# Kernel tuning notes

Measured on AMD Instinct MI355X. Metric: run time of the kernel, lower is better.

Reference implementation:

```python
import jax, jax.numpy as jnp
import numpy as np

EPS = 1e-8

def _rasterize_mesh(face_verts, H, W):
    # face_verts: [F,3,3] = (ndc_x, ndc_y, view_z) per triangle vertex
    x0, y0, z0 = face_verts[:, 0, 0], face_verts[:, 0, 1], face_verts[:, 0, 2]
    x1, y1, z1 = face_verts[:, 1, 0], face_verts[:, 1, 1], face_verts[:, 1, 2]
    x2, y2, z2 = face_verts[:, 2, 0], face_verts[:, 2, 1], face_verts[:, 2, 2]
    area = (x1 - x0) * (y2 - y0) - (y1 - y0) * (x2 - x0)
    # cull_backfaces=True (area<=0) + degenerate + behind-camera cull
    face_ok = (area > EPS) & (z0 > 0) & (z1 > 0) & (z2 > 0)
    inv_area = jnp.where(face_ok, 1.0 / jnp.where(face_ok, area, 1.0), 0.0)
    zs = jnp.stack([z0, z1, z2], -1)  # [F,3]
    # pytorch3d NDC: +x left, +y up, pixel centers
    xs = 1.0 - (2.0 * jnp.arange(W, dtype=jnp.float32) + 1.0) / W
    ys = 1.0 - (2.0 * jnp.arange(H, dtype=jnp.float32) + 1.0) / H

    def row_fn(py):
        px = xs[:, None]  # [W,1] broadcast vs faces [F]
        w0 = ((x1 - px) * (y2 - py) - (y1 - py) * (x2 - px)) * inv_area
        w1 = ((x2 - px) * (y0 - py) - (y2 - py) * (x0 - px)) * inv_area
        w2 = ((x0 - px) * (y1 - py) - (y0 - py) * (x1 - px)) * inv_area
        inside = (w0 >= 0) & (w1 >= 0) & (w2 >= 0) & face_ok
        # perspective_correct=True: l_i = w_i * prod(other z), renormalize
        l = jnp.stack([w0 * z1 * z2, z0 * w1 * z2, z0 * z1 * w2], -1)  # [W,F,3]
        s = l.sum(-1, keepdims=True)
        b = l / jnp.where(s == 0, 1.0, s)
        # clip_barycentric_coords=True
        b = jnp.clip(b, 0.0, None)
        b = b / jnp.clip(b.sum(-1, keepdims=True), EPS, None)
        zpix = (b * zs[None]).sum(-1)  # [W,F] interpolated view-space depth
        zm = jnp.where(inside, zpix, jnp.inf)
        fidx = jnp.argmin(zm, axis=1)  # z-buffer winner per pixel
        zmin = jnp.take_along_axis(zm, fidx[:, None], 1)[:, 0]
        hit = jnp.isfinite(zmin)
        bary = jnp.take_along_axis(b, fidx[:, None, None], 1)[:, 0]  # [W,3]
        return (jnp.where(hit, fidx, -1),
                jnp.where(hit, zmin, -1.0),
                jnp.where(hit[:, None], bary, -1.0))

    return jax.lax.map(row_fn, ys)  # ([H,W],[H,W],[H,W,3])


def _forward(positions, features, faces, K, RT, H, W):
    B, V, _ = positions.shape
    Fn = faces.shape[1]
    # --- create_camera_objects: open3d/opencv KRT -> pytorch3d camera ---
    R = RT[:, :, :3]
    t = RT[:, :, 3]
    scale = min(H, W) / 2.0
    focal = jnp.stack([K[:, 0, 0], K[:, 1, 1]], -1) / scale  # [B,2] NDC focal
    p0 = -(jnp.stack([K[:, 0, 2], K[:, 1, 2]], -1)
           - jnp.array([W / 2.0, H / 2.0], jnp.float32)) / scale  # [B,2]
    sign = jnp.array([-1.0, -1.0, 1.0], jnp.float32)
    R_p = jnp.swapaxes(R, 1, 2) * sign[None, None, :]  # R^T with cols 0,1 negated
    T_p = t * sign[None, :]
    # --- _get_mesh_ndc: world -> view -> NDC (pytorch3d row-vector convention) ---
    v_view = jnp.einsum('bvi,bij->bvj', positions, R_p) + T_p[:, None, :]
    z = v_view[..., 2:3]
    xy_ndc = focal[:, None, :] * v_view[..., :2] / z + p0[:, None, :]
    verts_ndc = jnp.concatenate([xy_ndc, z], -1)  # z overwritten with view-space depth
    face_verts = jax.vmap(lambda v, f: v[f])(verts_ndc, faces)  # [B,F,3,3]
    # --- rasterize (blur_sigma=0 -> faces_per_pixel=1) ---
    p2f, zbuf, bary = jax.vmap(lambda fv: _rasterize_mesh(fv, H, W))(face_verts)
    hit = p2f >= 0
    pix_to_face = jnp.where(hit, p2f + (jnp.arange(B) * Fn)[:, None, None], -1)
    # --- interpolate_face_attributes on packed faces/verts ---
    faces_packed = (faces + (jnp.arange(B) * V)[:, None, None]).reshape(B * Fn, 3)
    feats_packed = features.reshape(B * V, -1)
    fv_idx = faces_packed[jnp.clip(pix_to_face, 0)]  # [B,H,W,3]
    attrs = feats_packed[fv_idx]                      # [B,H,W,3,C]
    pix_feats = (bary[..., None] * attrs).sum(-2)
    pix_feats = jnp.where(hit[..., None], pix_feats, 0.0)
    dists = jnp.where(hit, 0.0, -1.0)
    # add faces_per_pixel (K=1) axis, matching pytorch3d Fragments layout
    return (pix_feats[:, :, :, None, :], pix_to_face[:, :, :, None],
            zbuf[:, :, :, None], bary[:, :, :, None, :], dists[:, :, :, None])


def setup_inputs() -> dict:
    key = jax.random.key(0)
    k1, k2, k3 = jax.random.split(key, 3)
    B, V, Fn, C, H, W = 1, 8192, 16384, 64, 192, 192
    positions = jax.random.uniform(k1, (B, V, 3), jnp.float32) * 2.0 - 1.0
    features = jax.random.normal(k2, (B, V, C), jnp.float32)
    faces = jax.random.randint(k3, (B, Fn, 3), 0, V)
    K = jnp.broadcast_to(jnp.array([[180.0, 0.0, 96.0], [0.0, 180.0, 96.0],
                                    [0.0, 0.0, 1.0]], jnp.float32), (B, 3, 3))
    RT = jnp.broadcast_to(jnp.concatenate(
        [jnp.eye(3, dtype=jnp.float32),
         jnp.array([[0.0], [0.0], [3.5]], jnp.float32)], axis=1), (B, 3, 4))
    return {"positions": positions, "features": features, "faces": faces,
            "K": K, "RT": RT, "H": H, "W": W, "blur_sigma": 0}


def reference(positions, features, faces, K, RT, H, W, blur_sigma):
    # blur_sigma == 0 path of VertexShader.forward (faces_per_pixel=1)
    return _forward(positions, features, faces, K, RT, H, W)
```

## Files before the change

kernel.cpp:

```cpp
#include <hip/hip_runtime.h>
#include <stdint.h>

#define H_ 192
#define W_ 192
#define C_ 64
#define EPS_F 1e-8f
#define TILE 16
#define NTX (W_/TILE)
#define NTY (H_/TILE)
#define CHUNK 256
#define NSLICE 8
#define NBUCKET 256
#define MAXCHUNK 64

typedef unsigned long long ull;

#define OFF_FEATS 0
#define OFF_P2F   (H_*W_*C_)
#define OFF_ZBUF  (OFF_P2F + H_*W_)
#define OFF_BARY  (OFF_ZBUF + H_*W_)
#define OFF_DIST  (OFF_BARY + H_*W_*3)

__device__ __forceinline__ float xm(float a, float b){ return __fmul_rn(a,b); }
__device__ __forceinline__ float xa(float a, float b){ return __fadd_rn(a,b); }
__device__ __forceinline__ float xsb(float a, float b){ return __fsub_rn(a,b); }
__device__ __forceinline__ float xd(float a, float b){ return __fdiv_rn(a,b); }

__device__ __forceinline__ float pixcoord(int i, float dim){
    float t = xa(xm(2.0f, (float)i), 1.0f);
    return xsb(1.0f, xd(t, dim));
}

__device__ __forceinline__ unsigned fenc(float f){
    unsigned b = __float_as_uint(f);
    return (b & 0x80000000u) ? ~b : (b | 0x80000000u);
}
__device__ __forceinline__ float fdec(unsigned e){
    unsigned b = (e & 0x80000000u) ? (e & 0x7FFFFFFFu) : ~e;
    return __uint_as_float(b);
}

__device__ __forceinline__ int zbucket(float zmn){
    int b = (int)((zmn - 2.0f) * 64.0f);
    return b < 0 ? 0 : (b > 254 ? 254 : b);
}
__device__ __forceinline__ float zlo_bucket(int b){
    if (b >= 255) return INFINITY;
    if (b == 0)   return 0.0f;
    return 2.0f + (float)b * 0.015625f;
}

__device__ __forceinline__ float3 tv(const float* __restrict__ pos,
        const float* __restrict__ K, const float* __restrict__ RT, int i){
    float p0 = pos[3*i+0], p1 = pos[3*i+1], p2 = pos[3*i+2];
    const float sgn[3] = {-1.f, -1.f, 1.f};
    float vv[3];
    #pragma unroll
    for (int j=0;j<3;j++){
        float rp0 = xm(RT[j*4+0], sgn[j]);
        float rp1 = xm(RT[j*4+1], sgn[j]);
        float rp2 = xm(RT[j*4+2], sgn[j]);
        float s = xa(xa(xm(p0,rp0), xm(p1,rp1)), xm(p2,rp2));
        vv[j] = xa(s, xm(RT[j*4+3], sgn[j]));
    }
    float z = vv[2];
    float fx = xd(K[0], 96.0f);
    float fy = xd(K[4], 96.0f);
    float p0x = -xd(xsb(K[2], 96.0f), 96.0f);
    float p0y = -xd(xsb(K[5], 96.0f), 96.0f);
    float xn = xa(xd(xm(fx, vv[0]), z), p0x);
    float yn = xa(xd(xm(fy, vv[1]), z), p0y);
    return make_float3(xn, yn, z);
}

__global__ __launch_bounds__(64) void k_pre(const float* __restrict__ pos,
        const float* __restrict__ K, const float* __restrict__ RT,
        const int* __restrict__ faces, float* __restrict__ rec0,
        unsigned* __restrict__ hist, unsigned* __restrict__ gbb,
        ull* __restrict__ keys, int Fn){
    __shared__ unsigned lh[NBUCKET];
    int t = threadIdx.x, B = blockIdx.x;
    int gthreads = gridDim.x*64;
    for (int i = B*64 + t; i < H_*W_; i += gthreads) keys[i] = 0xFFFFFFFFFFFFFFFFULL;
    #pragma unroll
    for (int i=t; i<NBUCKET; i+=64) lh[i] = 0u;
    __syncthreads();
    int f = B*64 + t;
    float bxmn=INFINITY, bxmx=-INFINITY, bymn=INFINITY, bymx=-INFINITY;
    if (f < Fn){
        int i0 = faces[3*f+0], i1 = faces[3*f+1], i2 = faces[3*f+2];
        float3 v0 = tv(pos,K,RT,i0), v1 = tv(pos,K,RT,i1), v2 = tv(pos,K,RT,i2);
        float area = xsb(xm(xsb(v1.x,v0.x), xsb(v2.y,v0.y)), xm(xsb(v1.y,v0.y), xsb(v2.x,v0.x)));
        bool ok = (area > EPS_F) && (v0.z > 0.f) && (v1.z > 0.f) && (v2.z > 0.f);
        float ia = ok ? xd(1.0f, area) : 0.0f;
        float zmn = INFINITY;
        int b = 255;
        if (ok){
            zmn = fminf(v0.z, fminf(v1.z, v2.z));
            b = zbucket(zmn);
            bxmn = fminf(v0.x, fminf(v1.x, v2.x)) - 1e-4f;
            bxmx = fmaxf(v0.x, fmaxf(v1.x, v2.x)) + 1e-4f;
            bymn = fminf(v0.y, fminf(v1.y, v2.y)) - 1e-4f;
            bymx = fmaxf(v0.y, fmaxf(v1.y, v2.y)) + 1e-4f;
        }
        atomicAdd(&lh[b], 1u);
        float4* q = (float4*)(rec0 + (size_t)f*12);
        q[0] = make_float4(v0.x, v0.y, v1.x, v1.y);
        q[1] = make_float4(v2.x, v2.y, v0.z, v1.z);
        q[2] = make_float4(v2.z, ia, __int_as_float(f), zmn);
    }
    #pragma unroll
    for (int s2=1; s2<64; s2<<=1){
        bxmn = fminf(bxmn, __shfl_xor(bxmn, s2, 64));
        bxmx = fmaxf(bxmx, __shfl_xor(bxmx, s2, 64));
        bymn = fminf(bymn, __shfl_xor(bymn, s2, 64));
        bymx = fmaxf(bymx, __shfl_xor(bymx, s2, 64));
    }
    if (t == 0 && bxmx > -INFINITY){
        atomicMax(&gbb[0], fenc(-bxmn));
        atomicMax(&gbb[1], fenc( bxmx));
        atomicMax(&gbb[2], fenc(-bymn));
        atomicMax(&gbb[3], fenc( bymx));
    }
    __syncthreads();
    #pragma unroll
    for (int i=t; i<NBUCKET; i+=64){
        unsigned cc = lh[i];
        if (cc) atomicAdd(&hist[i], cc);
    }
}

__global__ __launch_bounds__(256) void k_scatter(const float* __restrict__ rec0,
        const unsigned* __restrict__ hist, unsigned* __restrict__ histcur,
        float* __restrict__ rec, float* __restrict__ suffz, int Fn){
    __shared__ unsigned gst[NBUCKET], ssc[NBUCKET], lcnt[NBUCKET], lbase[NBUCKET];
    int t = threadIdx.x, B = blockIdx.x;
    unsigned hv = hist[t];
    ssc[t] = hv;
    lcnt[t] = 0u;
    __syncthreads();
    for (int d=1; d<NBUCKET; d<<=1){
        unsigned u = (t >= d) ? ssc[t-d] : 0u;
        __syncthreads();
        ssc[t] += u;
        __syncthreads();
    }
    gst[t] = ssc[t] - hv;
    __syncthreads();
    if (B == 0 && t < MAXCHUNK){
        unsigned pos = (unsigned)t * CHUNK;
        int bb = 0;
        #pragma unroll
        for (int s = 128; s > 0; s >>= 1){
            int nb = bb + s;
            if (nb <= NBUCKET && ssc[nb-1] <= pos) bb = nb;
        }
        suffz[t] = zlo_bucket(bb);
    }
    int f = B*256 + t;
    bool valid = (f < Fn);
    float4 q0, q1, q2;
    int b = 255; unsigned rank = 0; bool ok = false; float zmn = INFINITY;
    if (valid){
        const float4* q = (const float4*)(rec0 + (size_t)f*12);
        q0 = q[0]; q1 = q[1]; q2 = q[2];
        ok = (q2.y > 0.f);
        zmn = q2.w;
        b = ok ? zbucket(zmn) : 255;
        rank = atomicAdd(&lcnt[b], 1u);
    }
    __syncthreads();
    unsigned add = lcnt[t];
    if (add) lbase[t] = atomicAdd(&histcur[t], add);
    __syncthreads();
    if (valid){
        float x0=q0.x, y0=q0.y, x1=q0.z, y1=q0.w;
        float x2=q1.x, y2=q1.y, z0=q1.z, z1=q1.w;
        float z2=q2.x, ia=q2.y;
        float xmn, xmx, ymn, ymx, Ap=0.f, Bp=0.f, Cp=0.f;
        if (ok){
            xmn = fminf(x0, fminf(x1, x2)) - 1e-4f;
            xmx = fmaxf(x0, fmaxf(x1, x2)) + 1e-4f;
            ymn = fminf(y0, fminf(y1, y2)) - 1e-4f;
            ymx = fmaxf(y0, fmaxf(y1, y2)) + 1e-4f;
            float iz0 = 1.f/z0, iz1 = 1.f/z1, iz2 = 1.f/z2;
            Ap = ia * ((y1-y2)*iz0 + (y2-y0)*iz1 + (y0-y1)*iz2);
            Bp = ia * ((x2-x1)*iz0 + (x0-x2)*iz1 + (x1-x0)*iz2);
            Cp = ia * ((x1*y2-x2*y1)*iz0 + (x2*y0-x0*y2)*iz1 + (x0*y1-x1*y0)*iz2);
        } else {
            xmn = INFINITY; xmx = -INFINITY; ymn = INFINITY; ymx = -INFINITY;
        }
        unsigned p = gst[b] + lbase[b] + rank;
        float4* qo = (float4*)(rec + (size_t)p*20);
        qo[0] = q0; qo[1] = q1; qo[2] = q2;
        qo[3] = make_float4(Ap, Bp, Cp, 0.f);
        qo[4] = make_float4(xmn, xmx, ymn, ymx);
    }
}

__global__ __launch_bounds__(256) void k_raster(const float* __restrict__ rec,
        const float* __restrict__ suffz, const unsigned* __restrict__ gbb,
        ull* __restrict__ keys, int Fn){
    __shared__ float lds[CHUNK*12];
    __shared__ float zl[CHUNK];
    __shared__ int   slist[CHUNK];
    __shared__ int   wcnt[4];
    __shared__ float suff[MAXCHUNK];
    int tid = threadIdx.x;
    int nchunk = (Fn + CHUNK - 1) / CHUNK;
    if (tid < MAXCHUNK) suff[tid] = suffz[tid];
    int ix = blockIdx.x*TILE + (tid & 15);
    int iy = blockIdx.y*TILE + (tid >> 4);
    int pix = iy*W_ + ix;
    float px = pixcoord(ix, (float)W_);
    float py = pixcoord(iy, (float)H_);
    float tx_hi = pixcoord(blockIdx.x*TILE,          (float)W_);
    float tx_lo = pixcoord(blockIdx.x*TILE + TILE-1, (float)W_);
    float ty_hi = pixcoord(blockIdx.y*TILE,          (float)H_);
    float ty_lo = pixcoord(blockIdx.y*TILE + TILE-1, (float)H_);
    float gx0 = -fdec(gbb[0]), gx1 = fdec(gbb[1]);
    float gy0 = -fdec(gbb[2]), gy1 = fdec(gbb[3]);
    bool alive = (px >= gx0) && (px <= gx1) && (py >= gy0) && (py <= gy1);
    int lane = tid & 63, wv = tid >> 6;

    float zcut = alive ? INFINITY : -INFINITY;
    ull localkey = 0xFFFFFFFFFFFFFFFFULL;
    ull published = 0xFFFFFFFFFFFFFFFFULL;
    __syncthreads();

    for (int c = (int)blockIdx.z; c < nchunk; c += NSLICE){
        ull g = __hip_atomic_load(&keys[pix], __ATOMIC_RELAXED, __HIP_MEMORY_SCOPE_AGENT);
        float zg = __uint_as_float((unsigned)(g >> 32));
        zcut = fminf(zcut, zg);
        float sc = (c < MAXCHUNK) ? suff[c] : 0.0f;
        int done = (!alive || !(xm(sc, 0.999f) < zcut)) ? 1 : 0;
        if (__syncthreads_and(done)) break;

        int fi = c*CHUNK + tid;
        float4 q0 = make_float4(0,0,0,0), q1 = q0, q2 = q0;
        bool keep = false;
        float zb = 0.f;
        if (fi < Fn){
            const float4* gq = (const float4*)(rec + (size_t)fi*20);
            q0 = gq[0]; q1 = gq[1]; q2 = gq[2];
            float4 q3 = gq[3], q4 = gq[4];
            keep = (q4.x <= tx_hi) && (q4.y >= tx_lo) && (q4.z <= ty_hi) && (q4.w >= ty_lo);
            if (keep){
                float ax = (q3.x > 0.f) ? tx_hi : tx_lo;
                float by = (q3.y > 0.f) ? ty_hi : ty_lo;
                float Nmax = q3.z + q3.x*ax + q3.y*by;
                float M = fabsf(q3.x*ax) + fabsf(q3.y*by) + fabsf(q3.z);
                float Nub = Nmax + 1e-5f*M + 1e-30f;
                if (Nub <= 0.f) keep = false;
                else zb = fmaxf(1.f/Nub, q2.w);
            }
        }
        float4* l = (float4*)(lds + tid*12);
        l[0] = q0; l[1] = q1; l[2] = q2;
        ull m = __ballot(keep);
        if (lane == 0) wcnt[wv] = __popcll(m);
        __syncthreads();
        int basecnt = 0;
        #pragma unroll
        for (int w2 = 0; w2 < 4; ++w2) if (w2 < wv) basecnt += wcnt[w2];
        if (keep){
            int p = basecnt + __popcll(m & ((1ULL << lane) - 1ULL));
            slist[p] = tid;
            zl[p] = zb;
        }
        int nsurv = wcnt[0] + wcnt[1] + wcnt[2] + wcnt[3];
        __syncthreads();

        float zcmax = zcut;
        #pragma unroll
        for (int s2=1; s2<64; s2<<=1) zcmax = fmaxf(zcmax, __shfl_xor(zcmax, s2, 64));

        for (int k0 = 0; k0 < nsurv; k0 += 64){
            int kk = k0 + lane;
            float zlk = (kk < nsurv) ? zl[kk] : INFINITY;
            ull wm = __ballot(xm(zlk, 0.999f) < zcmax);
            while (wm){
                int k = (int)__ffsll(wm) - 1;
                wm &= wm - 1;
                k += k0;
                float zbl = zl[k];
                if (xm(zbl, 0.999f) < zcut){
                    int j = slist[k];
                    const float* r = lds + j*12;
                    float x0=r[0], y0=r[1], x1=r[2], y1=r[3], x2=r[4], y2=r[5];
                    float dx0=xsb(x0,px), dx1=xsb(x1,px), dx2=xsb(x2,px);
                    float dy0=xsb(y0,py), dy1=xsb(y1,py), dy2=xsb(y2,py);
                    float e0 = xsb(xm(dx1,dy2), xm(dy1,dx2));
                    float e1 = xsb(xm(dx2,dy0), xm(dy2,dx0));
                    float e2 = xsb(xm(dx0,dy1), xm(dy0,dx1));
                    if (e0 >= 0.f && e1 >= 0.f && e2 >= 0.f){
                        float z0=r[6], z1=r[7], z2=r[8], ia=r[9];
                        float w0 = xm(e0, ia), w1 = xm(e1, ia), w2 = xm(e2, ia);
                        float l0 = xm(xm(w0,z1),z2);
                        float l1 = xm(xm(z0,w1),z2);
                        float l2 = xm(xm(z0,z1),w2);
                        float s  = xa(xa(l0,l1),l2);
                        float za = (l0*z0 + l1*z1 + l2*z2) / s;
                        if (za*0.99999f < zcut){
                            float dn = (s == 0.f) ? 1.0f : s;
                            float b0 = fmaxf(xd(l0,dn), 0.f);
                            float b1 = fmaxf(xd(l1,dn), 0.f);
                            float b2 = fmaxf(xd(l2,dn), 0.f);
                            float bs = fmaxf(xa(xa(b0,b1),b2), EPS_F);
                            b0 = xd(b0,bs); b1 = xd(b1,bs); b2 = xd(b2,bs);
                            float zp = xa(xa(xm(b0,z0),xm(b1,z1)),xm(b2,z2));
                            ull ck = (((ull)__float_as_uint(zp)) << 32) | (unsigned)__float_as_int(r[10]);
                            if (ck < localkey) localkey = ck;
                            zcut = fminf(zcut, zp);
                        }
                    }
                }
            }
        }
        if (localkey < published){
            atomicMin(&keys[pix], localkey);
            published = localkey;
        }
    }
    if (localkey < published) atomicMin(&keys[pix], localkey);
}

__global__ __launch_bounds__(256) void k_post(const ull* __restrict__ keys,
        const float* __restrict__ rec0, const float* __restrict__ feats,
        const int* __restrict__ faces, float* __restrict__ out){
    int grp = threadIdx.x >> 6;
    int c = threadIdx.x & 63;
    int pix = blockIdx.x*4 + grp;
    float* p2f  = out + OFF_P2F;
    float* zbuf = out + OFF_ZBUF;
    float* bary = out + OFF_BARY;
    float* dist = out + OFF_DIST;
    ull key = keys[pix];
    if (key == 0xFFFFFFFFFFFFFFFFULL){
        out[OFF_FEATS + pix*C_ + c] = 0.0f;
        if (c == 0){
            p2f[pix] = -1.0f; zbuf[pix] = -1.0f; dist[pix] = -1.0f;
        }
        if (c < 3) bary[3*pix+c] = -1.0f;
        return;
    }
    int f = (int)(key & 0xFFFFFFFFu);
    float z = __uint_as_float((unsigned)(key >> 32));
    int ix = pix % W_, iy = pix / W_;
    float px = pixcoord(ix, (float)W_);
    float py = pixcoord(iy, (float)H_);
    const float4* q = (const float4*)(rec0 + (size_t)f*12);
    float4 q0 = q[0], q1 = q[1], q2 = q[2];
    float x0=q0.x, y0=q0.y, x1=q0.z, y1=q0.w;
    float x2=q1.x, y2=q1.y, z0=q1.z, z1=q1.w;
    float z2=q2.x, ia=q2.y;
    float w0 = xm(xsb(xm(xsb(x1,px),xsb(y2,py)), xm(xsb(y1,py),xsb(x2,px))), ia);
    float w1 = xm(xsb(xm(xsb(x2,px),xsb(y0,py)), xm(xsb(y2,py),xsb(x0,px))), ia);
    float w2 = xm(xsb(xm(xsb(x0,px),xsb(y1,py)), xm(xsb(y0,py),xsb(x1,px))), ia);
    float l0 = xm(xm(w0,z1),z2);
    float l1 = xm(xm(z0,w1),z2);
    float l2 = xm(xm(z0,z1),w2);
    float s  = xa(xa(l0,l1),l2);
    float dn = (s == 0.f) ? 1.0f : s;
    float b0 = fmaxf(xd(l0,dn), 0.f);
    float b1 = fmaxf(xd(l1,dn), 0.f);
    float b2 = fmaxf(xd(l2,dn), 0.f);
    float bs = fmaxf(xa(xa(b0,b1),b2), EPS_F);
    b0 = xd(b0,bs); b1 = xd(b1,bs); b2 = xd(b2,bs);
    int i0 = faces[3*f+0], i1 = faces[3*f+1], i2 = faces[3*f+2];
    float res = xa(xa(xm(b0, feats[i0*C_ + c]), xm(b1, feats[i1*C_ + c])),
                   xm(b2, feats[i2*C_ + c]));
    out[OFF_FEATS + pix*C_ + c] = res;
    if (c == 0){
        p2f[pix] = (float)f; zbuf[pix] = z; dist[pix] = 0.0f;
    }
    if (c < 3){
        float bb = (c == 0) ? b0 : ((c == 1) ? b1 : b2);
        bary[3*pix+c] = bb;
    }
}

extern "C" void kernel_launch(void* const* d_in, const int* in_sizes, int n_in,
                              void* d_out, int out_size, void* d_ws, size_t ws_size,
                              hipStream_t stream) {
    const float* positions = (const float*)d_in[0];
    const float* features  = (const float*)d_in[1];
    const int*   faces     = (const int*)  d_in[2];
    const float* K         = (const float*)d_in[3];
    const float* RT        = (const float*)d_in[4];
    int Fn = in_sizes[2] / 3;

    ull*      keys     = (ull*)d_ws;
    unsigned* hist     = (unsigned*)(keys + H_*W_);
    unsigned* histcur  = hist + NBUCKET;
    unsigned* gbb      = histcur + NBUCKET;
    float*    suffz    = (float*)(gbb + 4);
    float*    rec      = suffz + MAXCHUNK;
    float*    rec0     = rec + (size_t)Fn*20;

    size_t regB = (NBUCKET*2 + 4)*4;
    hipMemsetAsync(hist, 0x00, regB, stream);

    int nfb = (Fn + 255) / 256;
    k_pre<<<(Fn+63)/64, 64, 0, stream>>>(positions, K, RT, faces, rec0, hist, gbb, keys, Fn);
    k_scatter<<<nfb, 256, 0, stream>>>(rec0, hist, histcur, rec, suffz, Fn);
    dim3 rg(NTX, NTY, NSLICE);
    k_raster<<<rg, dim3(256,1,1), 0, stream>>>(rec, suffz, gbb, keys, Fn);
    k_post<<<(H_*W_)/4, 256, 0, stream>>>(keys, rec0, features, faces, (float*)d_out);
}
```

Measured before the change: 141.9 us.

## Prefetch next face chunk and cull with per-wave and per-pixel depth-plane bounds

```diff
diff --git a/kernel.cpp b/kernel.cpp
--- a/kernel.cpp
+++ b/kernel.cpp
@@ -203,6 +203,7 @@
         ull* __restrict__ keys, int Fn){
     __shared__ float lds[CHUNK*12];
     __shared__ float zl[CHUNK];
+    __shared__ float pA[CHUNK], pB[CHUNK], pC[CHUNK], pM[CHUNK];
     __shared__ int   slist[CHUNK];
     __shared__ int   wcnt[4];
     __shared__ float suff[MAXCHUNK];
@@ -218,17 +219,32 @@
     float tx_lo = pixcoord(blockIdx.x*TILE + TILE-1, (float)W_);
     float ty_hi = pixcoord(blockIdx.y*TILE,          (float)H_);
     float ty_lo = pixcoord(blockIdx.y*TILE + TILE-1, (float)H_);
+    float axmax = fmaxf(fabsf(tx_lo), fabsf(tx_hi));
+    float bymax = fmaxf(fabsf(ty_lo), fabsf(ty_hi));
     float gx0 = -fdec(gbb[0]), gx1 = fdec(gbb[1]);
     float gy0 = -fdec(gbb[2]), gy1 = fdec(gbb[3]);
     bool alive = (px >= gx0) && (px <= gx1) && (py >= gy0) && (py <= gy1);
     int lane = tid & 63, wv = tid >> 6;
+    float py_hi_w = pixcoord(blockIdx.y*TILE + wv*4,     (float)H_);
+    float py_lo_w = pixcoord(blockIdx.y*TILE + wv*4 + 3, (float)H_);
 
     float zcut = alive ? INFINITY : -INFINITY;
     ull localkey = 0xFFFFFFFFFFFFFFFFULL;
     ull published = 0xFFFFFFFFFFFFFFFFULL;
     __syncthreads();
 
-    for (int c = (int)blockIdx.z; c < nchunk; c += NSLICE){
+    int c = (int)blockIdx.z;
+    float4 r0, r1, r2, r3, r4;
+    r0 = r1 = r2 = r3 = r4 = make_float4(0,0,0,0);
+    if (c < nchunk){
+        int fi = c*CHUNK + tid;
+        if (fi < Fn){
+            const float4* gq = (const float4*)(rec + (size_t)fi*20);
+            r0 = gq[0]; r1 = gq[1]; r2 = gq[2]; r3 = gq[3]; r4 = gq[4];
+        }
+    }
+
+    while (c < nchunk){
         ull g = __hip_atomic_load(&keys[pix], __ATOMIC_RELAXED, __HIP_MEMORY_SCOPE_AGENT);
         float zg = __uint_as_float((unsigned)(g >> 32));
         zcut = fminf(zcut, zg);
@@ -237,26 +253,22 @@
         if (__syncthreads_and(done)) break;
 
         int fi = c*CHUNK + tid;
-        float4 q0 = make_float4(0,0,0,0), q1 = q0, q2 = q0;
         bool keep = false;
-        float zb = 0.f;
+        float zb = 0.f, Ap = 0.f, Bp = 0.f, Cp = 0.f, Me = 0.f;
         if (fi < Fn){
-            const float4* gq = (const float4*)(rec + (size_t)fi*20);
-            q0 = gq[0]; q1 = gq[1]; q2 = gq[2];
-            float4 q3 = gq[3], q4 = gq[4];
-            keep = (q4.x <= tx_hi) && (q4.y >= tx_lo) && (q4.z <= ty_hi) && (q4.w >= ty_lo);
+            keep = (r4.x <= tx_hi) && (r4.y >= tx_lo) && (r4.z <= ty_hi) && (r4.w >= ty_lo);
             if (keep){
-                float ax = (q3.x > 0.f) ? tx_hi : tx_lo;
-                float by = (q3.y > 0.f) ? ty_hi : ty_lo;
-                float Nmax = q3.z + q3.x*ax + q3.y*by;
-                float M = fabsf(q3.x*ax) + fabsf(q3.y*by) + fabsf(q3.z);
-                float Nub = Nmax + 1e-5f*M + 1e-30f;
-                if (Nub <= 0.f) keep = false;
-                else zb = fmaxf(1.f/Nub, q2.w);
+                Ap = r3.x; Bp = r3.y; Cp = r3.z;
+                Me = 1e-5f*(fabsf(Ap)*axmax + fabsf(Bp)*bymax + fabsf(Cp)) + 1e-30f;
+                float ax = (Ap > 0.f) ? tx_hi : tx_lo;
+                float by = (Bp > 0.f) ? ty_hi : ty_lo;
+                float Nub = Cp + Ap*ax + Bp*by + Me;
+                if (!(Nub > 0.f)) keep = false;
+                else zb = fmaxf(1.f/Nub, r2.w);
             }
         }
         float4* l = (float4*)(lds + tid*12);
-        l[0] = q0; l[1] = q1; l[2] = q2;
+        l[0] = r0; l[1] = r1; l[2] = r2;
         ull m = __ballot(keep);
         if (lane == 0) wcnt[wv] = __popcll(m);
         __syncthreads();
@@ -267,9 +279,19 @@
             int p = basecnt + __popcll(m & ((1ULL << lane) - 1ULL));
             slist[p] = tid;
             zl[p] = zb;
+            pA[p] = Ap; pB[p] = Bp; pC[p] = Cp; pM[p] = Me;
         }
         int nsurv = wcnt[0] + wcnt[1] + wcnt[2] + wcnt[3];
         __syncthreads();
+
+        int cn = c + NSLICE;
+        if (cn < nchunk){
+            int fj = cn*CHUNK + tid;
+            if (fj < Fn){
+                const float4* gq = (const float4*)(rec + (size_t)fj*20);
+                r0 = gq[0]; r1 = gq[1]; r2 = gq[2]; r3 = gq[3]; r4 = gq[4];
+            }
+        }
 
         float zcmax = zcut;
         #pragma unroll
@@ -277,43 +299,51 @@
 
         for (int k0 = 0; k0 < nsurv; k0 += 64){
             int kk = k0 + lane;
-            float zlk = (kk < nsurv) ? zl[kk] : INFINITY;
-            ull wm = __ballot(xm(zlk, 0.999f) < zcmax);
+            bool maybe = false;
+            if (kk < nsurv){
+                float A = pA[kk], Bc = pB[kk], Cc = pC[kk];
+                float ax = (A  > 0.f) ? tx_hi  : tx_lo;
+                float by = (Bc > 0.f) ? py_hi_w : py_lo_w;
+                float Nub = Cc + A*ax + Bc*by + pM[kk];
+                bool skip_plane = !(Nub > 0.f) || !(zcmax*Nub > 0.999f);
+                bool skip_zl = !(xm(zl[kk], 0.999f) < zcmax);
+                maybe = !skip_plane && !skip_zl;
+            }
+            ull wm = __ballot(maybe);
             while (wm){
                 int k = (int)__ffsll(wm) - 1;
                 wm &= wm - 1;
                 k += k0;
-                float zbl = zl[k];
-                if (xm(zbl, 0.999f) < zcut){
-                    int j = slist[k];
-                    const float* r = lds + j*12;
-                    float x0=r[0], y0=r[1], x1=r[2], y1=r[3], x2=r[4], y2=r[5];
-                    float dx0=xsb(x0,px), dx1=xsb(x1,px), dx2=xsb(x2,px);
-                    float dy0=xsb(y0,py), dy1=xsb(y1,py), dy2=xsb(y2,py);
-                    float e0 = xsb(xm(dx1,dy2), xm(dy1,dx2));
-                    float e1 = xsb(xm(dx2,dy0), xm(dy2,dx0));
-                    float e2 = xsb(xm(dx0,dy1), xm(dy0,dx1));
-                    if (e0 >= 0.f && e1 >= 0.f && e2 >= 0.f){
-                        float z0=r[6], z1=r[7], z2=r[8], ia=r[9];
-                        float w0 = xm(e0, ia), w1 = xm(e1, ia), w2 = xm(e2, ia);
-                        float l0 = xm(xm(w0,z1),z2);
-                        float l1 = xm(xm(z0,w1),z2);
-                        float l2 = xm(xm(z0,z1),w2);
-                        float s  = xa(xa(l0,l1),l2);
-                        float za = (l0*z0 + l1*z1 + l2*z2) / s;
-                        if (za*0.99999f < zcut){
-                            float dn = (s == 0.f) ? 1.0f : s;
-                            float b0 = fmaxf(xd(l0,dn), 0.f);
-                            float b1 = fmaxf(xd(l1,dn), 0.f);
-                            float b2 = fmaxf(xd(l2,dn), 0.f);
-                            float bs = fmaxf(xa(xa(b0,b1),b2), EPS_F);
-                            b0 = xd(b0,bs); b1 = xd(b1,bs); b2 = xd(b2,bs);
-                            float zp = xa(xa(xm(b0,z0),xm(b1,z1)),xm(b2,z2));
-                            ull ck = (((ull)__float_as_uint(zp)) << 32) | (unsigned)__float_as_int(r[10]);
-                            if (ck < localkey) localkey = ck;
-                            zcut = fminf(zcut, zp);
-                        }
-                    }
+                if (!(xm(zl[k], 0.999f) < zcut)) continue;
+                float A = pA[k], Bc = pB[k], Cc = pC[k];
+                float Nub = Cc + A*px + Bc*py + pM[k];
+                if (!(Nub > 0.f)) continue;
+                if (!(zcut*Nub > 0.999f)) continue;
+                int j = slist[k];
+                const float* r = lds + j*12;
+                float x0=r[0], y0=r[1], x1=r[2], y1=r[3], x2=r[4], y2=r[5];
+                float dx0=xsb(x0,px), dx1=xsb(x1,px), dx2=xsb(x2,px);
+                float dy0=xsb(y0,py), dy1=xsb(y1,py), dy2=xsb(y2,py);
+                float e0 = xsb(xm(dx1,dy2), xm(dy1,dx2));
+                float e1 = xsb(xm(dx2,dy0), xm(dy2,dx0));
+                float e2 = xsb(xm(dx0,dy1), xm(dy0,dx1));
+                if (e0 >= 0.f && e1 >= 0.f && e2 >= 0.f){
+                    float z0=r[6], z1=r[7], z2=r[8], ia=r[9];
+                    float w0 = xm(e0, ia), w1 = xm(e1, ia), w2 = xm(e2, ia);
+                    float l0 = xm(xm(w0,z1),z2);
+                    float l1 = xm(xm(z0,w1),z2);
+                    float l2 = xm(xm(z0,z1),w2);
+                    float s  = xa(xa(l0,l1),l2);
+                    float dn = (s == 0.f) ? 1.0f : s;
+                    float b0 = fmaxf(xd(l0,dn), 0.f);
+                    float b1 = fmaxf(xd(l1,dn), 0.f);
+                    float b2 = fmaxf(xd(l2,dn), 0.f);
+                    float bs = fmaxf(xa(xa(b0,b1),b2), EPS_F);
+                    b0 = xd(b0,bs); b1 = xd(b1,bs); b2 = xd(b2,bs);
+                    float zp = xa(xa(xm(b0,z0),xm(b1,z1)),xm(b2,z2));
+                    ull ck = (((ull)__float_as_uint(zp)) << 32) | (unsigned)__float_as_int(r[10]);
+                    if (ck < localkey) localkey = ck;
+                    zcut = fminf(zcut, zp);
                 }
             }
         }
@@ -321,6 +351,7 @@
             atomicMin(&keys[pix], localkey);
             published = localkey;
         }
+        c = cn;
     }
     if (localkey < published) atomicMin(&keys[pix], localkey);
 }
```

Result: no change. 144.1 us (+1.5%).
